# Kernel optimization log

Measured on AMD Instinct MI355X. Metric: run time of the kernel, lower is better.

The kernel has to match this reference:

```python
import jax, jax.numpy as jnp
import numpy as np

B, T = 64, 2048
RNN_H, EMB, ATT, N_FILT, K = 1024, 512, 128, 32, 31
PAD = (K - 1) // 2


def setup_inputs() -> dict:
    key = jax.random.key(0)
    ks = jax.random.split(key, 9)
    return {
        "hidden_atten_state": jax.random.normal(ks[0], (B, RNN_H), jnp.float32),
        "memory": jax.random.normal(ks[1], (B, T, EMB), jnp.float32),
        "memory_after": jax.random.normal(ks[2], (B, T, ATT), jnp.float32),
        "cumulative_attention_weights": jax.random.uniform(ks[3], (B, 2, T), jnp.float32),
        "mask": jax.random.randint(ks[4], (B, T), 0, 2) > 0,
        # learned params (torch Linear weight convention: [out, in]; conv: [O, I, K])
        "W_dec": jax.random.normal(ks[5], (ATT, RNN_H), jnp.float32) * 0.02,
        "W_conv": jax.random.normal(ks[6], (N_FILT, 2, K), jnp.float32) * 0.02,
        "W_loc": jax.random.normal(ks[7], (ATT, N_FILT), jnp.float32) * 0.02,
        "W_energy": jax.random.normal(ks[8], (1, ATT), jnp.float32) * 0.02,
    }


def reference(hidden_atten_state, memory, memory_after,
              cumulative_attention_weights, mask,
              W_dec, W_conv, W_loc, W_energy):
    # location features: conv1d [B,2,T] -> [B,N_FILT,T], no bias
    loc = jax.lax.conv_general_dilated(
        cumulative_attention_weights, W_conv,
        window_strides=(1,), padding=[(PAD, PAD)],
        dimension_numbers=("NCH", "OIH", "NCH"))
    # transpose(1,2) then linear N_FILT -> ATT: [B,T,ATT]
    after_weights = jnp.einsum("bct,ac->bta", loc, W_loc)
    # decoder query projection: [B,ATT], broadcast over T
    after_query = hidden_atten_state @ W_dec.T  # [B,ATT]
    # additive energies -> scalar per (b,t)
    e = jnp.tanh(after_query[:, None, :] + after_weights + memory_after)
    energies = jnp.einsum("bta,oa->bt", e, W_energy)  # o==1, squeezed
    energies = jnp.where(mask, -jnp.inf, energies)
    weights = jax.nn.softmax(energies, axis=1)  # [B,T]
    context = jnp.einsum("bt,btd->bd", weights, memory)  # bmm squeeze
    return context, weights
```

## Files before the change

### kernel.cpp

```cpp
#include <hip/hip_runtime.h>
#include <math.h>

#define B      64
#define T      2048
#define RNN_H  1024
#define EMB    512
#define ATT    128
#define NF     32
#define KW     31
#define PADW   15

#define TT  64
#define CW  (TT + KW - 1)

__global__ __launch_bounds__(256) void k_query(const float* __restrict__ hidden,
                                               const float* __restrict__ Wdec,
                                               float* __restrict__ aq) {
    int gw   = (blockIdx.x * blockDim.x + threadIdx.x) >> 6;
    int lane = threadIdx.x & 63;
    int b = gw >> 7, a = gw & (ATT - 1);
    const float4* h = (const float4*)(hidden + b * RNN_H);
    const float4* w = (const float4*)(Wdec   + a * RNN_H);
    float acc = 0.f;
#pragma unroll
    for (int i = 0; i < RNN_H / 4 / 64; ++i) {
        float4 hv = h[lane + i * 64];
        float4 wv = w[lane + i * 64];
        acc += hv.x * wv.x + hv.y * wv.y + hv.z * wv.z + hv.w * wv.w;
    }
#pragma unroll
    for (int off = 32; off; off >>= 1) acc += __shfl_down(acc, off);
    if (lane == 0) aq[gw] = acc;
}

__global__ __launch_bounds__(256) void k_energy(
    const float* __restrict__ cum,
    const float* __restrict__ mem_after,
    const int*   __restrict__ mask,
    const float* __restrict__ Wconv,
    const float* __restrict__ Wloc,
    const float* __restrict__ Wenergy,
    const float* __restrict__ aq,
    float* __restrict__ energies)
{
    __shared__ float cum_s[2][CW];
    __shared__ float wconv_s[NF * 2 * KW];
    __shared__ float wloc_s[NF * ATT];
    __shared__ float wen_s[ATT];
    __shared__ float aq_s[ATT];
    __shared__ float loc_s[NF * TT];

    int tid = threadIdx.x;
    int b   = blockIdx.x >> 5;
    int tc  = blockIdx.x & 31;
    int t0  = tc * TT;

    for (int i = tid; i < NF * 2 * KW; i += 256) wconv_s[i] = Wconv[i];
    for (int i = tid; i < NF * ATT; i += 256) {
        int c = i >> 7, a = i & (ATT - 1);
        wloc_s[i] = Wloc[a * NF + c];
    }
    if (tid < ATT) { wen_s[tid] = Wenergy[tid]; aq_s[tid] = aq[b * ATT + tid]; }
    for (int i = tid; i < 2 * CW; i += 256) {
        int ch = i / CW, j = i - ch * CW;
        int t  = t0 + j - PADW;
        cum_s[ch][j] = (t >= 0 && t < T) ? cum[(b * 2 + ch) * T + t] : 0.f;
    }
    __syncthreads();

    for (int i = tid; i < NF * TT; i += 256) {
        int c = i >> 6, tl = i & 63;
        const float* wc = &wconv_s[c * 2 * KW];
        float acc = 0.f;
#pragma unroll
        for (int k = 0; k < KW; ++k) {
            acc += cum_s[0][tl + k] * wc[k];
            acc += cum_s[1][tl + k] * wc[KW + k];
        }
        loc_s[i] = acc;
    }
    __syncthreads();

    int wv = tid >> 6, lane = tid & 63;
    const float2* wloc2 = (const float2*)wloc_s;
    float2 aq2 = ((const float2*)aq_s)[lane];
    float2 we2 = ((const float2*)wen_s)[lane];

    for (int tl = wv * 16; tl < wv * 16 + 16; ++tl) {
        int t = t0 + tl;
        float2 ma = ((const float2*)(mem_after + (size_t)(b * T + t) * ATT))[lane];
        float ax = 0.f, ay = 0.f;
#pragma unroll
        for (int c = 0; c < NF; ++c) {
            float  l  = loc_s[c * TT + tl];
            float2 wl = wloc2[c * (ATT / 2) + lane];
            ax += l * wl.x; ay += l * wl.y;
        }
        float e0 = tanhf(aq2.x + ax + ma.x);
        float e1 = tanhf(aq2.y + ay + ma.y);
        float s  = we2.x * e0 + we2.y * e1;
#pragma unroll
        for (int off = 32; off; off >>= 1) s += __shfl_down(s, off);
        if (lane == 0)
            energies[b * T + t] = mask[b * T + t] ? -INFINITY : s;
    }
}

__global__ __launch_bounds__(256) void k_softmax(float* __restrict__ w,
                                                 float* __restrict__ ctx) {
    int b = blockIdx.x, tid = threadIdx.x;
    ((float2*)(ctx + b * EMB))[tid] = make_float2(0.f, 0.f);

    float* row = w + b * T;
    float e[8];
    float m = -INFINITY;
#pragma unroll
    for (int j = 0; j < 8; ++j) { e[j] = row[tid + j * 256]; m = fmaxf(m, e[j]); }

    __shared__ float redm[4], reds[4];
#pragma unroll
    for (int off = 32; off; off >>= 1) m = fmaxf(m, __shfl_xor(m, off));
    if ((tid & 63) == 0) redm[tid >> 6] = m;
    __syncthreads();
    m = fmaxf(fmaxf(redm[0], redm[1]), fmaxf(redm[2], redm[3]));

    float s = 0.f;
#pragma unroll
    for (int j = 0; j < 8; ++j) { e[j] = expf(e[j] - m); s += e[j]; }
#pragma unroll
    for (int off = 32; off; off >>= 1) s += __shfl_xor(s, off);
    if ((tid & 63) == 0) reds[tid >> 6] = s;
    __syncthreads();
    s = reds[0] + reds[1] + reds[2] + reds[3];

    float inv = 1.f / s;
#pragma unroll
    for (int j = 0; j < 8; ++j) row[tid + j * 256] = e[j] * inv;
}

__global__ __launch_bounds__(128) void k_context(const float* __restrict__ memory,
                                                 const float* __restrict__ w,
                                                 float* __restrict__ ctx) {
    __shared__ float ws[64];
    int b = blockIdx.x >> 5, tc = blockIdx.x & 31;
    int t0 = tc * 64, tid = threadIdx.x;
    if (tid < 64) ws[tid] = w[b * T + t0 + tid];
    __syncthreads();

    const float4* mem4 = (const float4*)memory + (size_t)(b * T + t0) * (EMB / 4);
    float4 acc = make_float4(0.f, 0.f, 0.f, 0.f);
#pragma unroll 8
    for (int t = 0; t < 64; ++t) {
        float  wt = ws[t];
        float4 m  = mem4[(size_t)t * (EMB / 4) + tid];
        acc.x += wt * m.x; acc.y += wt * m.y; acc.z += wt * m.z; acc.w += wt * m.w;
    }
    float* dst = ctx + b * EMB + tid * 4;
    atomicAdd(dst + 0, acc.x);
    atomicAdd(dst + 1, acc.y);
    atomicAdd(dst + 2, acc.z);
    atomicAdd(dst + 3, acc.w);
}

extern "C" void kernel_launch(void* const* d_in, const int* in_sizes, int n_in,
                              void* d_out, int out_size, void* d_ws, size_t ws_size,
                              hipStream_t stream) {
    const float* hidden    = (const float*)d_in[0];
    const float* memory    = (const float*)d_in[1];
    const float* mem_after = (const float*)d_in[2];
    const float* cum       = (const float*)d_in[3];
    const int*   mask      = (const int*)  d_in[4];
    const float* Wdec      = (const float*)d_in[5];
    const float* Wconv     = (const float*)d_in[6];
    const float* Wloc      = (const float*)d_in[7];
    const float* Wenergy   = (const float*)d_in[8];

    float* ctx = (float*)d_out;
    float* wts = (float*)d_out + B * EMB;
    float* aq  = (float*)d_ws;

    k_query<<<(B * ATT) / 4, 256, 0, stream>>>(hidden, Wdec, aq);

    k_energy<<<B * (T / TT), 256, 0, stream>>>(cum, mem_after, mask, Wconv, Wloc,
                                               Wenergy, aq, wts);

    k_softmax<<<B, 256, 0, stream>>>(wts, ctx);

    k_context<<<B * (T / 64), 128, 0, stream>>>(memory, wts, ctx);
}
```

Measured before the change: 478.8 us.

## Fuse softmax into context kernel and use fast exp-based tanh

Merges the softmax and context kernels into one launch. Each of the 32 blocks per batch row redundantly recomputes the row max and sum from energies kept in workspace, then normalizes only its own 64-wide chunk before the weighted memory reduction. Zeroing of the context output moves into the energy kernel. tanhf and expf are replaced by __expf-based versions, which removes a launch and a round trip over the weights but adds redundant row reductions and some loss of accuracy.

```diff
diff --git a/kernel.cpp b/kernel.cpp
--- a/kernel.cpp
+++ b/kernel.cpp
@@ -12,6 +12,12 @@
 
 #define TT  64
 #define CW  (TT + KW - 1)
+
+__device__ __forceinline__ float fast_tanh(float x) {
+    x = fminf(fmaxf(x, -15.f), 15.f);
+    float e = __expf(2.f * x);
+    return (e - 1.f) / (e + 1.f);
+}
 
 __global__ __launch_bounds__(256) void k_query(const float* __restrict__ hidden,
                                                const float* __restrict__ Wdec,
@@ -41,7 +47,8 @@
     const float* __restrict__ Wloc,
     const float* __restrict__ Wenergy,
     const float* __restrict__ aq,
-    float* __restrict__ energies)
+    float* __restrict__ en,
+    float* __restrict__ ctx)
 {
     __shared__ float cum_s[2][CW];
     __shared__ float wconv_s[NF * 2 * KW];
@@ -54,6 +61,8 @@
     int b   = blockIdx.x >> 5;
     int tc  = blockIdx.x & 31;
     int t0  = tc * TT;
+
+    if (tid < 16) ctx[b * EMB + tc * 16 + tid] = 0.f;
 
     for (int i = tid; i < NF * 2 * KW; i += 256) wconv_s[i] = Wconv[i];
     for (int i = tid; i < NF * ATT; i += 256) {
@@ -96,64 +105,61 @@
             float2 wl = wloc2[c * (ATT / 2) + lane];
             ax += l * wl.x; ay += l * wl.y;
         }
-        float e0 = tanhf(aq2.x + ax + ma.x);
-        float e1 = tanhf(aq2.y + ay + ma.y);
+        float e0 = fast_tanh(aq2.x + ax + ma.x);
+        float e1 = fast_tanh(aq2.y + ay + ma.y);
         float s  = we2.x * e0 + we2.y * e1;
 #pragma unroll
         for (int off = 32; off; off >>= 1) s += __shfl_down(s, off);
         if (lane == 0)
-            energies[b * T + t] = mask[b * T + t] ? -INFINITY : s;
+            en[b * T + t] = mask[b * T + t] ? -INFINITY : s;
     }
 }
 
-__global__ __launch_bounds__(256) void k_softmax(float* __restrict__ w,
-                                                 float* __restrict__ ctx) {
-    int b = blockIdx.x, tid = threadIdx.x;
-    ((float2*)(ctx + b * EMB))[tid] = make_float2(0.f, 0.f);
+__global__ __launch_bounds__(128) void k_softmax_ctx(
+    const float* __restrict__ en,
+    const float* __restrict__ memory,
+    float* __restrict__ wts,
+    float* __restrict__ ctx)
+{
+    __shared__ float redm[2], reds[2];
+    __shared__ float ws_[64];
+    int b = blockIdx.x >> 5, tc = blockIdx.x & 31;
+    int t0 = tc * 64, tid = threadIdx.x;
 
-    float* row = w + b * T;
-    float e[8];
+    const float* row = en + b * T;
+    float e[16];
     float m = -INFINITY;
 #pragma unroll
-    for (int j = 0; j < 8; ++j) { e[j] = row[tid + j * 256]; m = fmaxf(m, e[j]); }
-
-    __shared__ float redm[4], reds[4];
+    for (int j = 0; j < 16; ++j) { e[j] = row[tid + j * 128]; m = fmaxf(m, e[j]); }
 #pragma unroll
     for (int off = 32; off; off >>= 1) m = fmaxf(m, __shfl_xor(m, off));
     if ((tid & 63) == 0) redm[tid >> 6] = m;
     __syncthreads();
-    m = fmaxf(fmaxf(redm[0], redm[1]), fmaxf(redm[2], redm[3]));
+    m = fmaxf(redm[0], redm[1]);
 
     float s = 0.f;
 #pragma unroll
-    for (int j = 0; j < 8; ++j) { e[j] = expf(e[j] - m); s += e[j]; }
+    for (int j = 0; j < 16; ++j) s += __expf(e[j] - m);
 #pragma unroll
     for (int off = 32; off; off >>= 1) s += __shfl_xor(s, off);
     if ((tid & 63) == 0) reds[tid >> 6] = s;
     __syncthreads();
-    s = reds[0] + reds[1] + reds[2] + reds[3];
+    float inv = 1.f / (reds[0] + reds[1]);
 
-    float inv = 1.f / s;
-#pragma unroll
-    for (int j = 0; j < 8; ++j) row[tid + j * 256] = e[j] * inv;
-}
-
-__global__ __launch_bounds__(128) void k_context(const float* __restrict__ memory,
-                                                 const float* __restrict__ w,
-                                                 float* __restrict__ ctx) {
-    __shared__ float ws[64];
-    int b = blockIdx.x >> 5, tc = blockIdx.x & 31;
-    int t0 = tc * 64, tid = threadIdx.x;
-    if (tid < 64) ws[tid] = w[b * T + t0 + tid];
+    if (tid < 64) {
+        float w = __expf(row[t0 + tid] - m) * inv;
+        wts[b * T + t0 + tid] = w;
+        ws_[tid] = w;
+    }
     __syncthreads();
 
     const float4* mem4 = (const float4*)memory + (size_t)(b * T + t0) * (EMB / 4);
     float4 acc = make_float4(0.f, 0.f, 0.f, 0.f);
 #pragma unroll 8
     for (int t = 0; t < 64; ++t) {
-        float  wt = ws[t];
-        float4 m  = mem4[(size_t)t * (EMB / 4) + tid];
-        acc.x += wt * m.x; acc.y += wt * m.y; acc.z += wt * m.z; acc.w += wt * m.w;
+        float  wt = ws_[t];
+        float4 mv = mem4[(size_t)t * (EMB / 4) + tid];
+        acc.x += wt * mv.x; acc.y += wt * mv.y; acc.z += wt * mv.z; acc.w += wt * mv.w;
     }
     float* dst = ctx + b * EMB + tid * 4;
     atomicAdd(dst + 0, acc.x);
@@ -178,13 +184,12 @@
     float* ctx = (float*)d_out;
     float* wts = (float*)d_out + B * EMB;
     float* aq  = (float*)d_ws;
+    float* en  = (float*)d_ws + B * ATT;
 
     k_query<<<(B * ATT) / 4, 256, 0, stream>>>(hidden, Wdec, aq);
 
     k_energy<<<B * (T / TT), 256, 0, stream>>>(cum, mem_after, mask, Wconv, Wloc,
-                                               Wenergy, aq, wts);
+                                               Wenergy, aq, en, ctx);
 
-    k_softmax<<<B, 256, 0, stream>>>(wts, ctx);
-
-    k_context<<<B * (T / 64), 128, 0, stream>>>(memory, wts, ctx);
+    k_softmax_ctx<<<B * (T / 64), 128, 0, stream>>>(en, memory, wts, ctx);
 }
```

Result: no change. 476.4 us (-0.5%).
